# Performance work log

Measured on AMD Instinct MI355X. Metric: run time of the kernel, lower is better.

The kernel has to match this reference:

```python
import jax, jax.numpy as jnp
import numpy as np

FS = 256  # sampling_rate
BANDS = [(0.5, 45.0), (0.5, 4.0), (4.0, 8.0), (8.0, 13.0), (13.0, 30.0), (30.0, 45.0)]
EPS = 1e-8


def _bandpass(sig, lo, hi):
    # FFT-domain brick-wall bandpass, matching bandpass_filter_fft
    T = sig.shape[-1]
    F = jnp.fft.rfft(sig, axis=-1)
    freqs = np.fft.rfftfreq(T, d=1.0 / FS)
    mask = jnp.asarray(((freqs >= lo) & (freqs <= hi)).astype(np.float32))
    return jnp.fft.irfft(F * mask, n=T, axis=-1)


def _phase(sig):
    # Hilbert transform -> instantaneous phase
    T = sig.shape[-1]
    h = np.zeros(T, np.float32)
    if T % 2 == 0:
        h[0] = 1.0; h[T // 2] = 1.0; h[1:T // 2] = 2.0
    else:
        h[0] = 1.0; h[1:(T + 1) // 2] = 2.0
    analytic = jnp.fft.ifft(jnp.fft.fft(sig, axis=-1) * jnp.asarray(h), axis=-1)
    return jnp.angle(analytic)


def _zscore(x):
    # matches torch: (x - mean) / (std_unbiased + 1e-8)
    m = x.mean(-1, keepdims=True)
    s = jnp.std(x, axis=-1, keepdims=True, ddof=1)
    return (x - m) / (s + EPS)


def _band_feats(e1, e2, lo, hi):
    B, C, T = e1.shape
    f1 = _bandpass(e1, lo, hi)
    f2 = _bandpass(e2, lo, hi)
    p1 = f1 ** 2
    p2 = f2 ** 2
    ph1 = _phase(f1)
    ph2 = _phase(f2)

    # PLV = |mean_t exp(i(phi1_i - phi2_j))| -> complex matmul over T
    z1 = jnp.exp(1j * ph1)                       # (B,C,T) complex64
    z2c = jnp.exp(-1j * ph2)
    plv = jnp.abs(jnp.einsum('bit,bjt->bij', z1, z2c)) / T

    # pairwise phase differences (B,C,C,T) -- honors the original full CxC structure
    pd = ph1[:, :, None, :] - ph2[:, None, :, :]
    s = jnp.sign(pd)
    pli = jnp.abs(s.mean(-1))

    # wPLI: power-weighted sign, weights normalized over T per (i,j)
    w = (p1[:, :, None, :] + p2[:, None, :, :]) * 0.5
    wn = w / (w.sum(-1, keepdims=True) + EPS)
    wpli = jnp.abs((s * wn).sum(-1))

    # Coherence: |X_i Y_j*|^2 / (|X_i|^2 |Y_j|^2 + eps), mean over freqs
    X1 = jnp.fft.rfft(f1, axis=-1)
    X2 = jnp.fft.rfft(f2, axis=-1)
    P1 = jnp.abs(X1) ** 2                        # (B,C,F)
    P2 = jnp.abs(X2) ** 2
    pw = P1[:, :, None, :] * P2[:, None, :, :]   # == |pxy|^2 == pxx*pyy
    coh = (pw / (pw + EPS)).mean(-1)

    # Power correlation: z-score over T then matmul / T
    pz1 = _zscore(p1)
    pz2 = _zscore(p2)
    pcorr = jnp.einsum('bit,bjt->bij', pz1, pz2) / T

    # Phase difference magnitude
    phdiff = jnp.abs(pd).mean(-1)

    # Time-domain correlation
    tz1 = _zscore(f1)
    tz2 = _zscore(f2)
    tcorr = jnp.einsum('bit,bjt->bij', tz1, tz2) / T

    # feature order: PLV, PLI, wPLI, Coherence, Power_Corr, Phase_Diff, Time_Corr
    return jnp.stack([plv, pli, wpli, coh, pcorr, phdiff, tcorr], axis=1)  # (B,7,C,C)


def setup_inputs() -> dict:
    key = jax.random.key(0)
    k1, k2 = jax.random.split(key)
    eeg1 = jax.random.normal(k1, (4, 64, 2048), dtype=jnp.float32)
    eeg2 = jax.random.normal(k2, (4, 64, 2048), dtype=jnp.float32)
    return {"eeg1": eeg1, "eeg2": eeg2}


def reference(eeg1, eeg2):
    # feature_type='all' -> all 7 features, 6 bands -> (B, 6, 7, C, C)
    feats = [_band_feats(eeg1, eeg2, lo, hi) for lo, hi in BANDS]
    return jnp.stack(feats, axis=1)
```

## Files before the change

### kernel.cpp

```cpp
#include <hip/hip_runtime.h>
#include <math.h>

__constant__ int c_klo[6] = {4, 4, 32, 64, 104, 240};
__constant__ int c_nk[6]  = {357, 29, 33, 41, 137, 121};

#define PI2_N 0.0030679615757712823f

__global__ __launch_bounds__(256) void k_twid(float2* __restrict__ twid) {
  int idx = blockIdx.x * 256 + threadIdx.x;
  int k = 4 + (idx >> 11);
  int t = idx & 2047;
  int m = (k * t) & 2047;
  float s, c;
  sincosf((float)m * PI2_N, &s, &c);
  twid[idx] = make_float2(c, s);
}

__global__ __launch_bounds__(256) void k_dft(const float* __restrict__ e1,
                                             const float* __restrict__ e2,
                                             float2* __restrict__ coef,
                                             float* __restrict__ pwr) {
  __shared__ float xs[2048];
  __shared__ float red[4][64][2];
  int sig = blockIdx.x;
  int b = sig >> 7, side = (sig >> 6) & 1, ch = sig & 63;
  int bside = b * 2 + side;
  const float* src = (side ? e2 : e1) + (size_t)(b * 64 + ch) * 2048;
  for (int q = 0; q < 2; ++q) {
    int i4 = q * 256 + threadIdx.x;
    ((float4*)xs)[i4] = ((const float4*)src)[i4];
  }
  __syncthreads();
  int binlane = threadIdx.x & 63, tch = threadIdx.x >> 6;
  int t0 = tch << 9;
  const float* xp = xs + t0;
  for (int rnd = 0; rnd < 6; ++rnd) {
    int kidx = rnd * 64 + binlane;
    int k = kidx + 4;
    float wr, wi, sr, si;
    sincosf(-(float)((k * t0) & 2047) * PI2_N, &wi, &wr);
    sincosf(-(float)k * PI2_N, &si, &sr);
    float are = 0.f, aim = 0.f;
    for (int tt = 0; tt < 512; tt += 4) {
      float4 xv = *(const float4*)(xp + tt);
      float nr, ni;
      are = fmaf(xv.x, wr, are); aim = fmaf(xv.x, wi, aim);
      nr = fmaf(wr, sr, -(wi * si)); ni = fmaf(wr, si, wi * sr); wr = nr; wi = ni;
      are = fmaf(xv.y, wr, are); aim = fmaf(xv.y, wi, aim);
      nr = fmaf(wr, sr, -(wi * si)); ni = fmaf(wr, si, wi * sr); wr = nr; wi = ni;
      are = fmaf(xv.z, wr, are); aim = fmaf(xv.z, wi, aim);
      nr = fmaf(wr, sr, -(wi * si)); ni = fmaf(wr, si, wi * sr); wr = nr; wi = ni;
      are = fmaf(xv.w, wr, are); aim = fmaf(xv.w, wi, aim);
      nr = fmaf(wr, sr, -(wi * si)); ni = fmaf(wr, si, wi * sr); wr = nr; wi = ni;
    }
    red[tch][binlane][0] = are;
    red[tch][binlane][1] = aim;
    __syncthreads();
    if (tch == 0 && kidx < 357) {
      float rr = red[0][binlane][0] + red[1][binlane][0] + red[2][binlane][0] + red[3][binlane][0];
      float ri = red[0][binlane][1] + red[1][binlane][1] + red[2][binlane][1] + red[3][binlane][1];
      int a = (bside * 357 + kidx) * 64 + ch;
      coef[a] = make_float2(rr, ri);
      pwr[a] = rr * rr + ri * ri;
    }
    __syncthreads();
  }
}

__global__ __launch_bounds__(256) void k_analytic(const float2* __restrict__ coef,
                                                  const float2* __restrict__ twid,
                                                  float* __restrict__ fields,
                                                  float* __restrict__ statp) {
  __shared__ float Fs[64 * 128];
  __shared__ float tws[64 * 64];
  int tchunk = blockIdx.x, bside = blockIdx.y, band = blockIdx.z;
  int ch = threadIdx.x & 63, tg = threadIdx.x >> 6;
  int kloB = c_klo[band], n = c_nk[band];
  int tbase = tchunk * 32;
  float ar[8], ai[8];
#pragma unroll
  for (int r = 0; r < 8; ++r) { ar[r] = 0.f; ai[r] = 0.f; }
  for (int c0 = 0; c0 < n; c0 += 64) {
    int kc = min(64, n - c0);
    int k0 = kloB + c0;
    int cbase = (bside * 357 + (k0 - 4)) * 64;
    for (int idx = threadIdx.x; idx < kc * 32; idx += 256)
      ((float4*)Fs)[idx] = ((const float4*)(coef + cbase))[idx];
    int tw0 = (k0 - 4) * 2048 + tbase;
    for (int idx = threadIdx.x; idx < kc * 32; idx += 256) {
      int kk = idx >> 5, tl = idx & 31;
      float2 v = twid[kk * 2048 + tw0 + tl];
      ((float2*)tws)[kk * 32 + tl] = v;
    }
    __syncthreads();
    const float* fp = Fs + ch * 2;
    const float4* twq = (const float4*)tws + tg * 4;
    for (int kk = 0; kk < kc; ++kk) {
      float Fre = fp[kk * 128], Fim = fp[kk * 128 + 1];
      float4 q0 = twq[kk * 16 + 0];
      float4 q1 = twq[kk * 16 + 1];
      float4 q2 = twq[kk * 16 + 2];
      float4 q3 = twq[kk * 16 + 3];
      ar[0] = fmaf(Fre, q0.x, fmaf(-Fim, q0.y, ar[0])); ai[0] = fmaf(Fre, q0.y, fmaf(Fim, q0.x, ai[0]));
      ar[1] = fmaf(Fre, q0.z, fmaf(-Fim, q0.w, ar[1])); ai[1] = fmaf(Fre, q0.w, fmaf(Fim, q0.z, ai[1]));
      ar[2] = fmaf(Fre, q1.x, fmaf(-Fim, q1.y, ar[2])); ai[2] = fmaf(Fre, q1.y, fmaf(Fim, q1.x, ai[2]));
      ar[3] = fmaf(Fre, q1.z, fmaf(-Fim, q1.w, ar[3])); ai[3] = fmaf(Fre, q1.w, fmaf(Fim, q1.z, ai[3]));
      ar[4] = fmaf(Fre, q2.x, fmaf(-Fim, q2.y, ar[4])); ai[4] = fmaf(Fre, q2.y, fmaf(Fim, q2.x, ai[4]));
      ar[5] = fmaf(Fre, q2.z, fmaf(-Fim, q2.w, ar[5])); ai[5] = fmaf(Fre, q2.w, fmaf(Fim, q2.z, ai[5]));
      ar[6] = fmaf(Fre, q3.x, fmaf(-Fim, q3.y, ar[6])); ai[6] = fmaf(Fre, q3.y, fmaf(Fim, q3.x, ai[6]));
      ar[7] = fmaf(Fre, q3.z, fmaf(-Fim, q3.w, ar[7])); ai[7] = fmaf(Fre, q3.w, fmaf(Fim, q3.z, ai[7]));
    }
    __syncthreads();
  }
  float sf = 0.f, sf2 = 0.f, sf4 = 0.f;
  int pbase = (band * 8 + bside) * 4;
  int toff = (tbase + tg * 8) * 64 + ch;
  float* fphi = fields + (size_t)(pbase + 0) * 131072 + toff;
  float* fcos = fields + (size_t)(pbase + 1) * 131072 + toff;
  float* fsin = fields + (size_t)(pbase + 2) * 131072 + toff;
  float* ffil = fields + (size_t)(pbase + 3) * 131072 + toff;
#pragma unroll
  for (int r = 0; r < 8; ++r) {
    float re = ar[r] * (1.f / 1024.f), im = ai[r] * (1.f / 1024.f);
    float mag2 = re * re + im * im;
    float rinv = mag2 > 0.f ? rsqrtf(mag2) : 0.f;
    float cc = mag2 > 0.f ? re * rinv : 1.f;
    float ss = im * rinv;
    float ph = atan2f(im, re);
    fphi[r * 64] = ph; fcos[r * 64] = cc; fsin[r * 64] = ss; ffil[r * 64] = re;
    float p = re * re;
    sf += re; sf2 += p; sf4 += p * p;
  }
  float* red = Fs;
  red[(tg * 64 + ch) * 3 + 0] = sf;
  red[(tg * 64 + ch) * 3 + 1] = sf2;
  red[(tg * 64 + ch) * 3 + 2] = sf4;
  __syncthreads();
  if (tg == 0) {
    float a0 = red[ch * 3] + red[(64 + ch) * 3] + red[(128 + ch) * 3] + red[(192 + ch) * 3];
    float a1 = red[ch * 3 + 1] + red[(64 + ch) * 3 + 1] + red[(128 + ch) * 3 + 1] + red[(192 + ch) * 3 + 1];
    float a2 = red[ch * 3 + 2] + red[(64 + ch) * 3 + 2] + red[(128 + ch) * 3 + 2] + red[(192 + ch) * 3 + 2];
    int o = (((band * 8 + bside) * 64 + tchunk) * 64 + ch) * 3;
    statp[o] = a0; statp[o + 1] = a1; statp[o + 2] = a2;
  }
}

__global__ __launch_bounds__(256) void k_statred(const float* __restrict__ statp,
                                                 float* __restrict__ stats) {
  int gid = blockIdx.x * 256 + threadIdx.x;
  int band = gid >> 9, bsd = (gid >> 6) & 7, ch = gid & 63;
  float s0 = 0.f, s1 = 0.f, s2 = 0.f;
  const float* p = statp + ((size_t)(band * 8 + bsd) * 64 * 64 + ch) * 3;
  for (int tc = 0; tc < 64; ++tc) { s0 += p[tc * 192]; s1 += p[tc * 192 + 1]; s2 += p[tc * 192 + 2]; }
  float* o = stats + (size_t)gid * 3;
  o[0] = s0; o[1] = s1; o[2] = s2;
}

__global__ __launch_bounds__(256) void k_pairs(const float* __restrict__ fields,
                                               float* __restrict__ part) {
  __shared__ float li[4 * 16 * 32];
  __shared__ float lj[4 * 16 * 64];
  int ts = blockIdx.x, itile = blockIdx.y, bb = blockIdx.z;
  int band = bb >> 2, b = bb & 3;
  int tid = threadIdx.x;
  int ti = tid >> 4, tj = tid & 15;
  const float* pi = fields + (size_t)((band * 8 + b * 2 + 0) * 4) * 131072;
  const float* pj = fields + (size_t)((band * 8 + b * 2 + 1) * 4) * 131072;
  float aP[2][4], aQ[2][4], aSg[2][4], aS1[2][4], aS2[2][4], aAp[2][4], aPp[2][4], aFf[2][4];
#pragma unroll
  for (int il = 0; il < 2; ++il)
#pragma unroll
    for (int jl = 0; jl < 4; ++jl) {
      aP[il][jl] = 0.f; aQ[il][jl] = 0.f; aSg[il][jl] = 0.f; aS1[il][jl] = 0.f;
      aS2[il][jl] = 0.f; aAp[il][jl] = 0.f; aPp[il][jl] = 0.f; aFf[il][jl] = 0.f;
    }
  int tb = ts * 128;
  for (int sub = 0; sub < 8; ++sub) {
    int t0 = tb + sub * 16;
#pragma unroll
    for (int q = 0; q < 2; ++q) {
      int fl = (q * 256 + tid) * 4;
      int f = fl >> 9, tt = (fl >> 5) & 15, cc = fl & 31;
      *(float4*)&li[fl] = *(const float4*)(pi + (size_t)f * 131072 + (t0 + tt) * 64 + itile * 32 + cc);
    }
#pragma unroll
    for (int q = 0; q < 4; ++q) {
      int fl = (q * 256 + tid) * 4;
      int f = fl >> 10, tt = (fl >> 6) & 15, cc = fl & 63;
      *(float4*)&lj[fl] = *(const float4*)(pj + (size_t)f * 131072 + (t0 + tt) * 64 + cc);
    }
    __syncthreads();
#pragma unroll 2
    for (int tt = 0; tt < 16; ++tt) {
      float2 ph1 = *(const float2*)&li[tt * 32 + ti * 2];
      float2 c1 = *(const float2*)&li[512 + tt * 32 + ti * 2];
      float2 s1 = *(const float2*)&li[1024 + tt * 32 + ti * 2];
      float2 f1 = *(const float2*)&li[1536 + tt * 32 + ti * 2];
      float4 ph2 = *(const float4*)&lj[tt * 64 + tj * 4];
      float4 c2 = *(const float4*)&lj[1024 + tt * 64 + tj * 4];
      float4 s2 = *(const float4*)&lj[2048 + tt * 64 + tj * 4];
      float4 f2 = *(const float4*)&lj[3072 + tt * 64 + tj * 4];
      float ph1a[2] = {ph1.x, ph1.y}, c1a[2] = {c1.x, c1.y}, s1a[2] = {s1.x, s1.y}, f1a[2] = {f1.x, f1.y};
      float ph2a[4] = {ph2.x, ph2.y, ph2.z, ph2.w};
      float c2a[4] = {c2.x, c2.y, c2.z, c2.w};
      float s2a[4] = {s2.x, s2.y, s2.z, s2.w};
      float f2a[4] = {f2.x, f2.y, f2.z, f2.w};
      float p1a[2] = {f1a[0] * f1a[0], f1a[1] * f1a[1]};
      float n1a[2] = {-p1a[0], -p1a[1]};
      float p2a[4] = {f2a[0] * f2a[0], f2a[1] * f2a[1], f2a[2] * f2a[2], f2a[3] * f2a[3]};
      float n2a[4] = {-p2a[0], -p2a[1], -p2a[2], -p2a[3]};
#pragma unroll
      for (int il = 0; il < 2; ++il) {
#pragma unroll
        for (int jl = 0; jl < 4; ++jl) {
          float pd = ph1a[il] - ph2a[jl];
          bool pos = pd > 0.f;
          aSg[il][jl] += pos ? 1.f : -1.f;
          aS1[il][jl] += pos ? p1a[il] : n1a[il];
          aS2[il][jl] += pos ? p2a[jl] : n2a[jl];
          aAp[il][jl] += fabsf(pd);
          aP[il][jl] = fmaf(c1a[il], c2a[jl], aP[il][jl]);
          aP[il][jl] = fmaf(s1a[il], s2a[jl], aP[il][jl]);
          aQ[il][jl] = fmaf(s1a[il], c2a[jl], aQ[il][jl]);
          aQ[il][jl] = fmaf(-c1a[il], s2a[jl], aQ[il][jl]);
          aPp[il][jl] = fmaf(p1a[il], p2a[jl], aPp[il][jl]);
          aFf[il][jl] = fmaf(f1a[il], f2a[jl], aFf[il][jl]);
        }
      }
    }
    __syncthreads();
  }
  int pb = (bb * 16 + ts) * 8;
#pragma unroll
  for (int il = 0; il < 2; ++il) {
    int ro = itile * 2048 + (ti * 2 + il) * 64 + tj * 4;
    *(float4*)&part[(size_t)(pb + 0) * 4096 + ro] = make_float4(aP[il][0], aP[il][1], aP[il][2], aP[il][3]);
    *(float4*)&part[(size_t)(pb + 1) * 4096 + ro] = make_float4(aQ[il][0], aQ[il][1], aQ[il][2], aQ[il][3]);
    *(float4*)&part[(size_t)(pb + 2) * 4096 + ro] = make_float4(aSg[il][0], aSg[il][1], aSg[il][2], aSg[il][3]);
    *(float4*)&part[(size_t)(pb + 3) * 4096 + ro] = make_float4(aS1[il][0], aS1[il][1], aS1[il][2], aS1[il][3]);
    *(float4*)&part[(size_t)(pb + 4) * 4096 + ro] = make_float4(aS2[il][0], aS2[il][1], aS2[il][2], aS2[il][3]);
    *(float4*)&part[(size_t)(pb + 5) * 4096 + ro] = make_float4(aAp[il][0], aAp[il][1], aAp[il][2], aAp[il][3]);
    *(float4*)&part[(size_t)(pb + 6) * 4096 + ro] = make_float4(aPp[il][0], aPp[il][1], aPp[il][2], aPp[il][3]);
    *(float4*)&part[(size_t)(pb + 7) * 4096 + ro] = make_float4(aFf[il][0], aFf[il][1], aFf[il][2], aFf[il][3]);
  }
}

__global__ __launch_bounds__(256) void k_final(const float* __restrict__ part,
                                               const float* __restrict__ stats,
                                               const float* __restrict__ pwr,
                                               float* __restrict__ out) {
  int gid = blockIdx.x * 256 + threadIdx.x;
  int bb = gid >> 12, rem = gid & 4095;
  int band = bb >> 2, b = bb & 3;
  int i = rem >> 6, j = rem & 63;
  float S[8];
#pragma unroll
  for (int a = 0; a < 8; ++a) S[a] = 0.f;
  const float* pp = part + (size_t)bb * 16 * 8 * 4096 + rem;
  for (int ts = 0; ts < 16; ++ts)
#pragma unroll
    for (int a = 0; a < 8; ++a) S[a] += pp[(ts * 8 + a) * 4096];
  const float* st1 = stats + (size_t)((band * 8 + b * 2 + 0) * 64 + i) * 3;
  const float* st2 = stats + (size_t)((band * 8 + b * 2 + 1) * 64 + j) * 3;
  float sf1 = st1[0], sp1 = st1[1], sq1 = st1[2];
  float sf2 = st2[0], sp2 = st2[1], sq2 = st2[2];
  const float T = 2048.f, Ti = 1.f / 2048.f, Vi = 1.f / 2047.f;
  float plv = sqrtf(S[0] * S[0] + S[1] * S[1]) * Ti;
  float pli = fabsf(S[2]) * Ti;
  float wpli = fabsf(0.5f * (S[3] + S[4])) / (0.5f * (sp1 + sp2) + 1e-8f);
  int kl = c_klo[band] - 4, n = c_nk[band];
  const float* P1 = pwr + ((b * 2 + 0) * 357 + kl) * 64 + i;
  const float* P2 = pwr + ((b * 2 + 1) * 357 + kl) * 64 + j;
  float coh = 0.f;
  for (int kk = 0; kk < n; ++kk) {
    float r = P1[kk * 64] * P2[kk * 64];
    coh += __fdividef(r, r + 1e-8f);
  }
  coh *= (1.f / 1025.f);
  float mp1 = sp1 * Ti, mp2 = sp2 * Ti;
  float sd1 = sqrtf(fmaxf((sq1 - T * mp1 * mp1) * Vi, 0.f));
  float sd2 = sqrtf(fmaxf((sq2 - T * mp2 * mp2) * Vi, 0.f));
  float pcorr = (S[6] - T * mp1 * mp2) / ((sd1 + 1e-8f) * (sd2 + 1e-8f)) * Ti;
  float phd = S[5] * Ti;
  float mf1 = sf1 * Ti, mf2 = sf2 * Ti;
  float se1 = sqrtf(fmaxf((sp1 - T * mf1 * mf1) * Vi, 0.f));
  float se2 = sqrtf(fmaxf((sp2 - T * mf2 * mf2) * Vi, 0.f));
  float tcorr = (S[7] - T * mf1 * mf2) / ((se1 + 1e-8f) * (se2 + 1e-8f)) * Ti;
  size_t ob = (size_t)((b * 6 + band) * 7) * 4096 + rem;
  out[ob] = plv;
  out[ob + 4096] = pli;
  out[ob + 2 * 4096] = wpli;
  out[ob + 3 * 4096] = coh;
  out[ob + 4 * 4096] = pcorr;
  out[ob + 5 * 4096] = phd;
  out[ob + 6 * 4096] = tcorr;
}

extern "C" void kernel_launch(void* const* d_in, const int* in_sizes, int n_in,
                              void* d_out, int out_size, void* d_ws, size_t ws_size,
                              hipStream_t stream) {
  const float* e1 = (const float*)d_in[0];
  const float* e2 = (const float*)d_in[1];
  float* out = (float*)d_out;
  char* ws = (char*)d_ws;
  size_t off = 0;
  auto alloc = [&](size_t bytes) -> void* {
    void* p = ws + off;
    off += (bytes + 255) & ~(size_t)255;
    return p;
  };
  float2* twid = (float2*)alloc((size_t)357 * 2048 * 8);
  float2* coef = (float2*)alloc((size_t)8 * 357 * 64 * 8);
  float* pwr = (float*)alloc((size_t)8 * 357 * 64 * 4);
  float* fields = (float*)alloc((size_t)6 * 8 * 4 * 2048 * 64 * 4);
  float* statp = (float*)alloc((size_t)6 * 8 * 64 * 64 * 3 * 4);
  float* stats = (float*)alloc((size_t)6 * 8 * 64 * 3 * 4);
  float* part = (float*)alloc((size_t)24 * 16 * 8 * 4096 * 4);
  (void)in_sizes; (void)n_in; (void)out_size; (void)ws_size;

  hipLaunchKernelGGL(k_twid, dim3(2856), dim3(256), 0, stream, twid);
  hipLaunchKernelGGL(k_dft, dim3(512), dim3(256), 0, stream, e1, e2, coef, pwr);
  hipLaunchKernelGGL(k_analytic, dim3(64, 8, 6), dim3(256), 0, stream, coef, twid, fields, statp);
  hipLaunchKernelGGL(k_statred, dim3(12), dim3(256), 0, stream, statp, stats);
  hipLaunchKernelGGL(k_pairs, dim3(16, 2, 24), dim3(256), 0, stream, fields, part);
  hipLaunchKernelGGL(k_final, dim3(384), dim3(256), 0, stream, part, stats, pwr, out);
}
```

Baseline: 331.8 us.

## Fuse band synthesis with on-the-fly twiddle recurrence and derive band 0 from sub-bands

Drops the precomputed twiddle table kernel and instead generates twiddles per thread with a complex rotation recurrence inside the inverse-DFT loop. One block now processes all bands for a time chunk. The full band 0 is built as the sum of bands 1-5 plus a correction for the shared boundary bin, so its long 357-bin sum is not recomputed. Stores go through an LDS transpose so global writes are coalesced float4. The sum and sum-of-squares statistics now come from the spectral power via Parseval (the mean of a bandpassed signal is zero), so only the fourth-moment partials are kept. The trade-offs are lower grid parallelism (256 blocks at one block per CU) and some float rounding drift from the twiddle recurrence and the changed summation order.

```diff
diff --git a/kernel.cpp b/kernel.cpp
--- a/kernel.cpp
+++ b/kernel.cpp
@@ -5,16 +5,6 @@
 __constant__ int c_nk[6]  = {357, 29, 33, 41, 137, 121};
 
 #define PI2_N 0.0030679615757712823f
-
-__global__ __launch_bounds__(256) void k_twid(float2* __restrict__ twid) {
-  int idx = blockIdx.x * 256 + threadIdx.x;
-  int k = 4 + (idx >> 11);
-  int t = idx & 2047;
-  int m = (k * t) & 2047;
-  float s, c;
-  sincosf((float)m * PI2_N, &s, &c);
-  twid[idx] = make_float2(c, s);
-}
 
 __global__ __launch_bounds__(256) void k_dft(const float* __restrict__ e1,
                                              const float* __restrict__ e2,
@@ -67,93 +57,135 @@
   }
 }
 
-__global__ __launch_bounds__(256) void k_analytic(const float2* __restrict__ coef,
-                                                  const float2* __restrict__ twid,
-                                                  float* __restrict__ fields,
-                                                  float* __restrict__ statp) {
-  __shared__ float Fs[64 * 128];
-  __shared__ float tws[64 * 64];
-  int tchunk = blockIdx.x, bside = blockIdx.y, band = blockIdx.z;
-  int ch = threadIdx.x & 63, tg = threadIdx.x >> 6;
-  int kloB = c_klo[band], n = c_nk[band];
-  int tbase = tchunk * 32;
-  float ar[8], ai[8];
-#pragma unroll
-  for (int r = 0; r < 8; ++r) { ar[r] = 0.f; ai[r] = 0.f; }
-  for (int c0 = 0; c0 < n; c0 += 64) {
-    int kc = min(64, n - c0);
-    int k0 = kloB + c0;
-    int cbase = (bside * 357 + (k0 - 4)) * 64;
-    for (int idx = threadIdx.x; idx < kc * 32; idx += 256)
-      ((float4*)Fs)[idx] = ((const float4*)(coef + cbase))[idx];
-    int tw0 = (k0 - 4) * 2048 + tbase;
-    for (int idx = threadIdx.x; idx < kc * 32; idx += 256) {
-      int kk = idx >> 5, tl = idx & 31;
-      float2 v = twid[kk * 2048 + tw0 + tl];
-      ((float2*)tws)[kk * 32 + tl] = v;
-    }
-    __syncthreads();
-    const float* fp = Fs + ch * 2;
-    const float4* twq = (const float4*)tws + tg * 4;
-    for (int kk = 0; kk < kc; ++kk) {
-      float Fre = fp[kk * 128], Fim = fp[kk * 128 + 1];
-      float4 q0 = twq[kk * 16 + 0];
-      float4 q1 = twq[kk * 16 + 1];
-      float4 q2 = twq[kk * 16 + 2];
-      float4 q3 = twq[kk * 16 + 3];
-      ar[0] = fmaf(Fre, q0.x, fmaf(-Fim, q0.y, ar[0])); ai[0] = fmaf(Fre, q0.y, fmaf(Fim, q0.x, ai[0]));
-      ar[1] = fmaf(Fre, q0.z, fmaf(-Fim, q0.w, ar[1])); ai[1] = fmaf(Fre, q0.w, fmaf(Fim, q0.z, ai[1]));
-      ar[2] = fmaf(Fre, q1.x, fmaf(-Fim, q1.y, ar[2])); ai[2] = fmaf(Fre, q1.y, fmaf(Fim, q1.x, ai[2]));
-      ar[3] = fmaf(Fre, q1.z, fmaf(-Fim, q1.w, ar[3])); ai[3] = fmaf(Fre, q1.w, fmaf(Fim, q1.z, ai[3]));
-      ar[4] = fmaf(Fre, q2.x, fmaf(-Fim, q2.y, ar[4])); ai[4] = fmaf(Fre, q2.y, fmaf(Fim, q2.x, ai[4]));
-      ar[5] = fmaf(Fre, q2.z, fmaf(-Fim, q2.w, ar[5])); ai[5] = fmaf(Fre, q2.w, fmaf(Fim, q2.z, ai[5]));
-      ar[6] = fmaf(Fre, q3.x, fmaf(-Fim, q3.y, ar[6])); ai[6] = fmaf(Fre, q3.y, fmaf(Fim, q3.x, ai[6]));
-      ar[7] = fmaf(Fre, q3.z, fmaf(-Fim, q3.w, ar[7])); ai[7] = fmaf(Fre, q3.w, fmaf(Fim, q3.z, ai[7]));
-    }
-    __syncthreads();
-  }
-  float sf = 0.f, sf2 = 0.f, sf4 = 0.f;
-  int pbase = (band * 8 + bside) * 4;
-  int toff = (tbase + tg * 8) * 64 + ch;
-  float* fphi = fields + (size_t)(pbase + 0) * 131072 + toff;
-  float* fcos = fields + (size_t)(pbase + 1) * 131072 + toff;
-  float* fsin = fields + (size_t)(pbase + 2) * 131072 + toff;
-  float* ffil = fields + (size_t)(pbase + 3) * 131072 + toff;
-#pragma unroll
-  for (int r = 0; r < 8; ++r) {
-    float re = ar[r] * (1.f / 1024.f), im = ai[r] * (1.f / 1024.f);
-    float mag2 = re * re + im * im;
-    float rinv = mag2 > 0.f ? rsqrtf(mag2) : 0.f;
-    float cc = mag2 > 0.f ? re * rinv : 1.f;
-    float ss = im * rinv;
-    float ph = atan2f(im, re);
-    fphi[r * 64] = ph; fcos[r * 64] = cc; fsin[r * 64] = ss; ffil[r * 64] = re;
-    float p = re * re;
-    sf += re; sf2 += p; sf4 += p * p;
-  }
-  float* red = Fs;
-  red[(tg * 64 + ch) * 3 + 0] = sf;
-  red[(tg * 64 + ch) * 3 + 1] = sf2;
-  red[(tg * 64 + ch) * 3 + 2] = sf4;
-  __syncthreads();
-  if (tg == 0) {
-    float a0 = red[ch * 3] + red[(64 + ch) * 3] + red[(128 + ch) * 3] + red[(192 + ch) * 3];
-    float a1 = red[ch * 3 + 1] + red[(64 + ch) * 3 + 1] + red[(128 + ch) * 3 + 1] + red[(192 + ch) * 3 + 1];
-    float a2 = red[ch * 3 + 2] + red[(64 + ch) * 3 + 2] + red[(128 + ch) * 3 + 2] + red[(192 + ch) * 3 + 2];
-    int o = (((band * 8 + bside) * 64 + tchunk) * 64 + ch) * 3;
-    statp[o] = a0; statp[o + 1] = a1; statp[o + 2] = a2;
-  }
-}
-
-__global__ __launch_bounds__(256) void k_statred(const float* __restrict__ statp,
+__global__ __launch_bounds__(256, 1) void k_analytic(const float2* __restrict__ coef,
+                                                     float* __restrict__ fields,
+                                                     float* __restrict__ statp4) {
+  __shared__ float Fs[65 * 128];
+  __shared__ float Ltr[4 * 64 * 65];
+  int tchunk = blockIdx.x, bside = blockIdx.y;
+  int lane = threadIdx.x & 63;
+  int wv = threadIdx.x >> 6;
+  int ch0 = wv * 16;
+  int t = tchunk * 64 + lane;
+  float Rr, Ri;
+  sincosf((float)t * PI2_N, &Ri, &Rr);
+  float asr[16], asi[16];
+#pragma unroll
+  for (int c = 0; c < 16; ++c) { asr[c] = 0.f; asi[c] = 0.f; }
+
+  auto emit = [&](int bb, const float (&xr)[16], const float (&xi)[16]) {
+#pragma unroll
+    for (int c = 0; c < 16; ++c) {
+      float re = xr[c] * (1.f / 1024.f);
+      float im = xi[c] * (1.f / 1024.f);
+      float mag2 = fmaf(re, re, im * im);
+      float rinv = mag2 > 0.f ? rsqrtf(mag2) : 0.f;
+      float cc = mag2 > 0.f ? re * rinv : 1.f;
+      float ss = im * rinv;
+      float ph = atan2f(im, re);
+      int ca = (ch0 + c) * 65 + lane;
+      Ltr[ca] = ph;
+      Ltr[4160 + ca] = cc;
+      Ltr[8320 + ca] = ss;
+      Ltr[12480 + ca] = re;
+    }
+    __syncthreads();
+    size_t pb = (size_t)((bb * 8 + bside) * 4) * 131072 + (size_t)tchunk * 4096;
+    for (int f = 0; f < 4; ++f) {
+      float* op = fields + pb + (size_t)f * 131072;
+      const float* lp = Ltr + f * 4160;
+      for (int idx = threadIdx.x; idx < 1024; idx += 256) {
+        int tt = idx >> 4;
+        int c4 = (idx & 15) * 4;
+        float4 v = make_float4(lp[(c4 + 0) * 65 + tt], lp[(c4 + 1) * 65 + tt],
+                               lp[(c4 + 2) * 65 + tt], lp[(c4 + 3) * 65 + tt]);
+        *(float4*)(op + tt * 64 + c4) = v;
+      }
+    }
+    if (threadIdx.x < 64) {
+      const float* lp = Ltr + 12480 + threadIdx.x * 65;
+      float s = 0.f;
+      for (int tt = 0; tt < 64; ++tt) { float v = lp[tt]; float p = v * v; s = fmaf(p, p, s); }
+      statp4[((bb * 8 + bside) * 32 + tchunk) * 64 + threadIdx.x] = s;
+    }
+    __syncthreads();
+  };
+
+  for (int bnd = 1; bnd <= 5; ++bnd) {
+    int klo = c_klo[bnd], nk = c_nk[bnd];
+    float ar_[16], ai_[16];
+#pragma unroll
+    for (int c = 0; c < 16; ++c) { ar_[c] = 0.f; ai_[c] = 0.f; }
+    float Wr, Wi;
+    { int m = (klo * t) & 2047; sincosf((float)m * PI2_N, &Wi, &Wr); }
+    for (int c0 = 0; c0 < nk; c0 += 64) {
+      int kc = min(64, nk - c0);
+      __syncthreads();
+      {
+        int cbase = (bside * 357 + (klo - 4) + c0) * 64;
+        const float4* srcp = (const float4*)(coef + cbase);
+        for (int idx = threadIdx.x; idx < kc * 32; idx += 256)
+          ((float4*)Fs)[idx] = srcp[idx];
+      }
+      __syncthreads();
+      if (c0 == 0 && bnd >= 2) {
+        const float4* Fk = ((const float4*)Fs) + (ch0 >> 1);
+#pragma unroll
+        for (int q = 0; q < 8; ++q) {
+          float4 F = Fk[q];
+          asr[2 * q]     = fmaf(-F.x, Wr, asr[2 * q]);     asr[2 * q]     = fmaf( F.y, Wi, asr[2 * q]);
+          asi[2 * q]     = fmaf(-F.x, Wi, asi[2 * q]);     asi[2 * q]     = fmaf(-F.y, Wr, asi[2 * q]);
+          asr[2 * q + 1] = fmaf(-F.z, Wr, asr[2 * q + 1]); asr[2 * q + 1] = fmaf( F.w, Wi, asr[2 * q + 1]);
+          asi[2 * q + 1] = fmaf(-F.z, Wi, asi[2 * q + 1]); asi[2 * q + 1] = fmaf(-F.w, Wr, asi[2 * q + 1]);
+        }
+      }
+      const float4* Fp = ((const float4*)Fs) + (ch0 >> 1);
+      float4 Fa[8];
+#pragma unroll
+      for (int q = 0; q < 8; ++q) Fa[q] = Fp[q];
+      for (int kk = 0; kk < kc; ++kk) {
+        float4 Fb[8];
+        const float4* Fn = Fp + 32;
+#pragma unroll
+        for (int q = 0; q < 8; ++q) Fb[q] = Fn[q];
+#pragma unroll
+        for (int q = 0; q < 8; ++q) {
+          float4 F = Fa[q];
+          ar_[2 * q]     = fmaf(F.x, Wr, ar_[2 * q]);     ar_[2 * q]     = fmaf(-F.y, Wi, ar_[2 * q]);
+          ai_[2 * q]     = fmaf(F.x, Wi, ai_[2 * q]);     ai_[2 * q]     = fmaf( F.y, Wr, ai_[2 * q]);
+          ar_[2 * q + 1] = fmaf(F.z, Wr, ar_[2 * q + 1]); ar_[2 * q + 1] = fmaf(-F.w, Wi, ar_[2 * q + 1]);
+          ai_[2 * q + 1] = fmaf(F.z, Wi, ai_[2 * q + 1]); ai_[2 * q + 1] = fmaf( F.w, Wr, ai_[2 * q + 1]);
+        }
+        float t0r = Wr * Rr, t1i = Wr * Ri;
+        Wr = fmaf(-Wi, Ri, t0r);
+        Wi = fmaf(Wi, Rr, t1i);
+#pragma unroll
+        for (int q = 0; q < 8; ++q) Fa[q] = Fb[q];
+        Fp += 32;
+      }
+    }
+#pragma unroll
+    for (int c = 0; c < 16; ++c) { asr[c] += ar_[c]; asi[c] += ai_[c]; }
+    emit(bnd, ar_, ai_);
+  }
+  emit(0, asr, asi);
+}
+
+__global__ __launch_bounds__(256) void k_statred(const float* __restrict__ statp4,
+                                                 const float* __restrict__ pwr,
                                                  float* __restrict__ stats) {
   int gid = blockIdx.x * 256 + threadIdx.x;
   int band = gid >> 9, bsd = (gid >> 6) & 7, ch = gid & 63;
-  float s0 = 0.f, s1 = 0.f, s2 = 0.f;
-  const float* p = statp + ((size_t)(band * 8 + bsd) * 64 * 64 + ch) * 3;
-  for (int tc = 0; tc < 64; ++tc) { s0 += p[tc * 192]; s1 += p[tc * 192 + 1]; s2 += p[tc * 192 + 2]; }
-  float* o = stats + (size_t)gid * 3;
-  o[0] = s0; o[1] = s1; o[2] = s2;
+  int klo = c_klo[band], nk = c_nk[band];
+  const float* pp = pwr + ((bsd * 357) + (klo - 4)) * 64 + ch;
+  float sp = 0.f;
+  for (int kk = 0; kk < nk; ++kk) sp += pp[kk * 64];
+  sp *= (1.f / 1024.f);
+  const float* qp = statp4 + (size_t)((band * 8 + bsd) * 32) * 64 + ch;
+  float sq = 0.f;
+  for (int tc = 0; tc < 32; ++tc) sq += qp[tc * 64];
+  stats[gid * 2] = sp;
+  stats[gid * 2 + 1] = sq;
 }
 
 __global__ __launch_bounds__(256) void k_pairs(const float* __restrict__ fields,
@@ -260,10 +292,10 @@
   for (int ts = 0; ts < 16; ++ts)
 #pragma unroll
     for (int a = 0; a < 8; ++a) S[a] += pp[(ts * 8 + a) * 4096];
-  const float* st1 = stats + (size_t)((band * 8 + b * 2 + 0) * 64 + i) * 3;
-  const float* st2 = stats + (size_t)((band * 8 + b * 2 + 1) * 64 + j) * 3;
-  float sf1 = st1[0], sp1 = st1[1], sq1 = st1[2];
-  float sf2 = st2[0], sp2 = st2[1], sq2 = st2[2];
+  const float* st1 = stats + (size_t)((band * 8 + b * 2 + 0) * 64 + i) * 2;
+  const float* st2 = stats + (size_t)((band * 8 + b * 2 + 1) * 64 + j) * 2;
+  float sp1 = st1[0], sq1 = st1[1];
+  float sp2 = st2[0], sq2 = st2[1];
   const float T = 2048.f, Ti = 1.f / 2048.f, Vi = 1.f / 2047.f;
   float plv = sqrtf(S[0] * S[0] + S[1] * S[1]) * Ti;
   float pli = fabsf(S[2]) * Ti;
@@ -282,10 +314,9 @@
   float sd2 = sqrtf(fmaxf((sq2 - T * mp2 * mp2) * Vi, 0.f));
   float pcorr = (S[6] - T * mp1 * mp2) / ((sd1 + 1e-8f) * (sd2 + 1e-8f)) * Ti;
   float phd = S[5] * Ti;
-  float mf1 = sf1 * Ti, mf2 = sf2 * Ti;
-  float se1 = sqrtf(fmaxf((sp1 - T * mf1 * mf1) * Vi, 0.f));
-  float se2 = sqrtf(fmaxf((sp2 - T * mf2 * mf2) * Vi, 0.f));
-  float tcorr = (S[7] - T * mf1 * mf2) / ((se1 + 1e-8f) * (se2 + 1e-8f)) * Ti;
+  float se1 = sqrtf(sp1 * Vi);
+  float se2 = sqrtf(sp2 * Vi);
+  float tcorr = S[7] / ((se1 + 1e-8f) * (se2 + 1e-8f)) * Ti;
   size_t ob = (size_t)((b * 6 + band) * 7) * 4096 + rem;
   out[ob] = plv;
   out[ob + 4096] = pli;
@@ -309,19 +340,17 @@
     off += (bytes + 255) & ~(size_t)255;
     return p;
   };
-  float2* twid = (float2*)alloc((size_t)357 * 2048 * 8);
   float2* coef = (float2*)alloc((size_t)8 * 357 * 64 * 8);
   float* pwr = (float*)alloc((size_t)8 * 357 * 64 * 4);
   float* fields = (float*)alloc((size_t)6 * 8 * 4 * 2048 * 64 * 4);
-  float* statp = (float*)alloc((size_t)6 * 8 * 64 * 64 * 3 * 4);
-  float* stats = (float*)alloc((size_t)6 * 8 * 64 * 3 * 4);
+  float* statp4 = (float*)alloc((size_t)6 * 8 * 32 * 64 * 4);
+  float* stats = (float*)alloc((size_t)6 * 8 * 64 * 2 * 4);
   float* part = (float*)alloc((size_t)24 * 16 * 8 * 4096 * 4);
   (void)in_sizes; (void)n_in; (void)out_size; (void)ws_size;
 
-  hipLaunchKernelGGL(k_twid, dim3(2856), dim3(256), 0, stream, twid);
   hipLaunchKernelGGL(k_dft, dim3(512), dim3(256), 0, stream, e1, e2, coef, pwr);
-  hipLaunchKernelGGL(k_analytic, dim3(64, 8, 6), dim3(256), 0, stream, coef, twid, fields, statp);
-  hipLaunchKernelGGL(k_statred, dim3(12), dim3(256), 0, stream, statp, stats);
+  hipLaunchKernelGGL(k_analytic, dim3(32, 8), dim3(256), 0, stream, coef, fields, statp4);
+  hipLaunchKernelGGL(k_statred, dim3(12), dim3(256), 0, stream, statp4, pwr, stats);
   hipLaunchKernelGGL(k_pairs, dim3(16, 2, 24), dim3(256), 0, stream, fields, part);
   hipLaunchKernelGGL(k_final, dim3(384), dim3(256), 0, stream, part, stats, pwr, out);
 }
```

After: 401.8 us. 21.1% more time.
